# Kernel optimization log

Measured on AMD Instinct MI355X. Metric: run time of the kernel, lower is better.

Reference implementation:

```python
import jax, jax.numpy as jnp
import numpy as np

B, QDIM, KDIM, EMBED, HEADS = 8, 256, 256, 512, 8
HIMG, WIMG = 32, 32
HEAD_DIM = EMBED // HEADS


def setup_inputs() -> dict:
    key = jax.random.key(0)
    ks = jax.random.split(key, 8)
    scale_q = 1.0 / np.sqrt(QDIM)
    scale_k = 1.0 / np.sqrt(KDIM)
    return {
        "query": jax.random.normal(ks[0], (B, QDIM, HIMG, WIMG), jnp.float32),
        "key": jax.random.normal(ks[1], (B, KDIM, HIMG, WIMG), jnp.float32),
        "Wq": jax.random.uniform(ks[2], (EMBED, QDIM), jnp.float32, -scale_q, scale_q),
        "bq": jax.random.uniform(ks[3], (EMBED,), jnp.float32, -scale_q, scale_q),
        "Wk": jax.random.uniform(ks[4], (EMBED, KDIM), jnp.float32, -scale_k, scale_k),
        "bk": jax.random.uniform(ks[5], (EMBED,), jnp.float32, -scale_k, scale_k),
        "Wv": jax.random.uniform(ks[6], (EMBED, KDIM), jnp.float32, -scale_k, scale_k),
        "bv": jax.random.uniform(ks[7], (EMBED,), jnp.float32, -scale_k, scale_k),
    }


def reference(query, key, Wq, bq, Wk, bk, Wv, bv):
    b, _, h, w = query.shape
    s = h * w
    # (B, C, H, W) -> (B, S, C)
    q = query.transpose(0, 2, 3, 1).reshape(b, s, QDIM)
    kv = key.transpose(0, 2, 3, 1).reshape(b, s, KDIM)
    q = q @ Wq.T + bq            # (B, S, E)
    k = kv @ Wk.T + bk
    v = kv @ Wv.T + bv
    # split heads: (B, S, H, D) -> (B, H, S, D)
    q = q.reshape(b, s, HEADS, HEAD_DIM).transpose(0, 2, 1, 3)
    k = k.reshape(b, s, HEADS, HEAD_DIM).transpose(0, 2, 1, 3)
    v = v.reshape(b, s, HEADS, HEAD_DIM).transpose(0, 2, 1, 3)
    scores = jnp.einsum("bhqd,bhkd->bhqk", q, k) / np.sqrt(HEAD_DIM)
    # causal additive mask: -inf above the diagonal
    causal = jnp.tril(jnp.ones((s, s), dtype=bool))
    scores = jnp.where(causal, scores, -jnp.inf)
    attn = jax.nn.softmax(scores, axis=-1)
    x = jnp.einsum("bhqk,bhkd->bhqd", attn, v)   # (B, H, S, D)
    # (B, H, S, D) -> (B, H, D, S) -> (B, E, H_img, W_img)
    out = x.transpose(0, 1, 3, 2).reshape(b, EMBED, h, w)
    return out
```

## Files before the change

kernel.cpp:

```cpp
#include <hip/hip_runtime.h>
#include <hip/hip_bf16.h>

#define BATCH 8
#define CDIM 256
#define SEQ 1024
#define EMB 512
#define NHEAD 8
#define HDIM 64

typedef __bf16 bf16x8 __attribute__((ext_vector_type(8)));
typedef float f32x4 __attribute__((ext_vector_type(4)));
typedef float f32x16 __attribute__((ext_vector_type(16)));

static __device__ __forceinline__ unsigned short f2b(float f) {
    __hip_bfloat16 h = __float2bfloat16(f);
    return __builtin_bit_cast(unsigned short, h);
}

static __device__ __forceinline__ f32x4 mfma16(bf16x8 a, bf16x8 b, f32x4 c) {
    return __builtin_amdgcn_mfma_f32_16x16x32_bf16(a, b, c, 0, 0, 0);
}
static __device__ __forceinline__ f32x16 mfma32(bf16x8 a, bf16x8 b, f32x16 c) {
    return __builtin_amdgcn_mfma_f32_32x32x16_bf16(a, b, c, 0, 0, 0);
}

__global__ __launch_bounds__(256) void prep_w(
    const float* __restrict__ Wq, const float* __restrict__ Wk,
    const float* __restrict__ Wv, unsigned short* __restrict__ Wc)
{
    int pz = blockIdx.z;
    const float* W = (pz == 0) ? Wq : (pz == 1 ? Wk : Wv);
    int idx = (blockIdx.x * 256 + threadIdx.x) * 8;
    float4 v0 = *(const float4*)&W[idx];
    float4 v1 = *(const float4*)&W[idx + 4];
    int4 pk;
    pk.x = (int)((unsigned)f2b(v0.x) | ((unsigned)f2b(v0.y) << 16));
    pk.y = (int)((unsigned)f2b(v0.z) | ((unsigned)f2b(v0.w) << 16));
    pk.z = (int)((unsigned)f2b(v1.x) | ((unsigned)f2b(v1.y) << 16));
    pk.w = (int)((unsigned)f2b(v1.z) | ((unsigned)f2b(v1.w) << 16));
    *(int4*)&Wc[(size_t)pz * (EMB * CDIM) + idx] = pk;
}

__global__ __launch_bounds__(256) void transpose_cvt(
    const float* __restrict__ query, const float* __restrict__ key_,
    unsigned short* __restrict__ Xq, unsigned short* __restrict__ Xk)
{
    __shared__ alignas(16) unsigned short sT[64 * 66];
    int tid = threadIdx.x;
    int s0 = blockIdx.x * 64, c0 = blockIdx.y * 64;
    int z = blockIdx.z;
    int which = z >> 3, b = z & 7;
    const float* src = which ? key_ : query;
    unsigned short* dst = which ? Xk : Xq;

#pragma unroll
    for (int p = 0; p < 4; ++p) {
        int c = (tid >> 4) + p * 16;
        int sch = tid & 15;
        float4 v = *(const float4*)&src[((size_t)b * CDIM + c0 + c) * SEQ + s0 + sch * 4];
        sT[c * 66 + sch * 4 + 0] = f2b(v.x);
        sT[c * 66 + sch * 4 + 1] = f2b(v.y);
        sT[c * 66 + sch * 4 + 2] = f2b(v.z);
        sT[c * 66 + sch * 4 + 3] = f2b(v.w);
    }
    __syncthreads();
#pragma unroll
    for (int p = 0; p < 4; ++p) {
        int s = (tid >> 4) + p * 16;
        int cch = tid & 15;
        unsigned short e0 = sT[(cch * 4 + 0) * 66 + s];
        unsigned short e1 = sT[(cch * 4 + 1) * 66 + s];
        unsigned short e2 = sT[(cch * 4 + 2) * 66 + s];
        unsigned short e3 = sT[(cch * 4 + 3) * 66 + s];
        uint2 pk;
        pk.x = (unsigned)e0 | ((unsigned)e1 << 16);
        pk.y = (unsigned)e2 | ((unsigned)e3 << 16);
        *(uint2*)&dst[((size_t)b * SEQ + s0 + s) * CDIM + c0 + cch * 4] = pk;
    }
}

__global__ __launch_bounds__(256) void proj_kernel(
    const unsigned short* __restrict__ Xq, const unsigned short* __restrict__ Xk,
    const unsigned short* __restrict__ Wc,
    const float* __restrict__ bq, const float* __restrict__ bk,
    const float* __restrict__ bv,
    unsigned short* __restrict__ Qb, unsigned short* __restrict__ Kb,
    unsigned short* __restrict__ Vt)
{
    __shared__ alignas(16) unsigned short sA[128 * 72];
    __shared__ alignas(16) unsigned short sB[128 * 72];
    int tid = threadIdx.x;
    int n0 = blockIdx.x * 128;
    int m0 = blockIdx.y * 128;
    int proj = n0 >> 9;
    const unsigned short* X = (proj == 0) ? Xq : Xk;
    const float* bias = (proj == 0) ? bq : (proj == 1 ? bk : bv);

    int lane = tid & 63, w = tid >> 6;
    int l16 = lane & 15, lhi = lane >> 4;
    int wr = w >> 1, wc = w & 1;

    f32x4 zero = {0.f, 0.f, 0.f, 0.f};
    f32x4 acc[4][4];
#pragma unroll
    for (int i = 0; i < 4; ++i)
#pragma unroll
        for (int j = 0; j < 4; ++j) acc[i][j] = zero;

    for (int kt = 0; kt < 4; ++kt) {
        int c0 = kt * 64;
        if (kt) __syncthreads();
#pragma unroll
        for (int p = 0; p < 4; ++p) {
            int row = (tid >> 3) + p * 32, ch = tid & 7;
            *(int4*)&sA[row * 72 + ch * 8] =
                *(const int4*)&X[(size_t)(m0 + row) * CDIM + c0 + ch * 8];
            *(int4*)&sB[row * 72 + ch * 8] =
                *(const int4*)&Wc[(size_t)(n0 + row) * CDIM + c0 + ch * 8];
        }
        __syncthreads();
        const unsigned short* tA = (proj == 2) ? &sB[0] : &sA[0];
        const unsigned short* tB = (proj == 2) ? &sA[0] : &sB[0];
#pragma unroll
        for (int kk = 0; kk < 2; ++kk) {
            bf16x8 af[4], bfr[4];
#pragma unroll
            for (int i = 0; i < 4; ++i)
                af[i] = *(const bf16x8*)&tA[(wr * 64 + i * 16 + l16) * 72 + kk * 32 + lhi * 8];
#pragma unroll
            for (int j = 0; j < 4; ++j)
                bfr[j] = *(const bf16x8*)&tB[(wc * 64 + j * 16 + l16) * 72 + kk * 32 + lhi * 8];
#pragma unroll
            for (int i = 0; i < 4; ++i)
#pragma unroll
                for (int j = 0; j < 4; ++j)
                    acc[i][j] = mfma16(af[i], bfr[j], acc[i][j]);
        }
    }

    if (proj != 2) {
        unsigned short* dst = proj ? Kb : Qb;
        float scale = proj ? 1.0f : (0.125f * 1.44269504f);
#pragma unroll
        for (int i = 0; i < 4; ++i) {
#pragma unroll
            for (int j = 0; j < 4; ++j) {
                int e = (n0 & 511) + wc * 64 + j * 16 + l16;
                float bval = bias[e];
                int hh = e >> 6, dd = e & 63;
#pragma unroll
                for (int r = 0; r < 4; ++r) {
                    int mg = m0 + wr * 64 + i * 16 + lhi * 4 + r;
                    int bb = mg >> 10, s = mg & 1023;
                    dst[(((size_t)bb * NHEAD + hh) * SEQ + s) * HDIM + dd] =
                        f2b((acc[i][j][r] + bval) * scale);
                }
            }
        }
    } else {
#pragma unroll
        for (int i = 0; i < 4; ++i) {
#pragma unroll
            for (int r = 0; r < 4; ++r) {
                int e = (n0 & 511) + wr * 64 + i * 16 + lhi * 4 + r;
                float bval = bias[e];
                int hh = e >> 6, dd = e & 63;
#pragma unroll
                for (int j = 0; j < 4; ++j) {
                    int mg = m0 + wc * 64 + j * 16 + l16;
                    int bb = mg >> 10, s = mg & 1023;
                    Vt[(((size_t)bb * NHEAD + hh) * HDIM + dd) * SEQ + s] =
                        f2b(acc[i][j][r] + bval);
                }
            }
        }
    }
}

__global__ __launch_bounds__(64, 3) void attn_kernel(
    const unsigned short* __restrict__ Qb, const unsigned short* __restrict__ Kb,
    const unsigned short* __restrict__ Vt, float* __restrict__ out)
{
    int lane = threadIdx.x;
    int l32 = lane & 31, hi = lane >> 5;
    int bh = blockIdx.x;
    int qt = (int)(gridDim.y - 1 - blockIdx.y);
    int b = bh >> 3, h = bh & 7;
    int q0 = qt * 32;

    const unsigned short* Qhead = Qb + (size_t)bh * SEQ * HDIM;
    const unsigned short* Khead = Kb + (size_t)bh * SEQ * HDIM;
    const unsigned short* Vhead = Vt + (size_t)bh * HDIM * SEQ;

    bf16x8 qf[4];
#pragma unroll
    for (int dblk = 0; dblk < 4; ++dblk)
        qf[dblk] = *(const bf16x8*)&Qhead[(size_t)(q0 + l32) * HDIM + dblk * 16 + hi * 8];

    f32x16 o0, o1;
#pragma unroll
    for (int r = 0; r < 16; ++r) { o0[r] = 0.f; o1[r] = 0.f; }
    float m = -1e30f, l = 0.f;

    int nt = qt + 1;
    for (int kt = 0; kt < nt; ++kt) {
        int k0 = kt * 32;
        bf16x8 ka[4];
#pragma unroll
        for (int dblk = 0; dblk < 4; ++dblk)
            ka[dblk] = *(const bf16x8*)&Khead[(size_t)(k0 + l32) * HDIM + dblk * 16 + hi * 8];
        f32x16 st;
#pragma unroll
        for (int r = 0; r < 16; ++r) st[r] = 0.f;
#pragma unroll
        for (int dblk = 0; dblk < 4; ++dblk)
            st = mfma32(ka[dblk], qf[dblk], st);

        bf16x8 va[2][2];
#pragma unroll
        for (int t = 0; t < 2; ++t)
#pragma unroll
            for (int ks = 0; ks < 2; ++ks)
                va[t][ks] = *(const bf16x8*)
                    &Vhead[(size_t)(t * 32 + l32) * SEQ + k0 + ks * 16 + hi * 8];

        if (kt == qt) {
#pragma unroll
            for (int r = 0; r < 16; ++r) {
                int kk = (r & 3) + 8 * (r >> 2) + 4 * hi;
                if (kk > l32) st[r] = -1e38f;
            }
        }

        float tmax = st[0];
#pragma unroll
        for (int r = 1; r < 16; ++r) tmax = fmaxf(tmax, st[r]);
        tmax = fmaxf(tmax, __shfl_xor(tmax, 32));
        if (!__all(tmax <= m + 8.0f)) {
            float mnew = fmaxf(m, tmax);
            float corr = __builtin_amdgcn_exp2f(m - mnew);
#pragma unroll
            for (int r = 0; r < 16; ++r) { o0[r] *= corr; o1[r] *= corr; }
            l *= corr;
            m = mnew;
        }
        float p[16];
        float ts = 0.f;
#pragma unroll
        for (int r = 0; r < 16; ++r) {
            p[r] = __builtin_amdgcn_exp2f(st[r] - m);
            ts += p[r];
        }
        ts += __shfl_xor(ts, 32);
        l += ts;

        unsigned u[8];
#pragma unroll
        for (int i = 0; i < 8; ++i) {
            unsigned r_;
            asm("v_cvt_pk_bf16_f32 %0, %1, %2" : "=v"(r_) : "v"(p[2 * i]), "v"(p[2 * i + 1]));
            u[i] = r_;
        }
        asm("v_permlane32_swap_b32 %0, %1" : "+v"(u[0]), "+v"(u[2]));
        asm("v_permlane32_swap_b32 %0, %1" : "+v"(u[1]), "+v"(u[3]));
        asm("v_permlane32_swap_b32 %0, %1" : "+v"(u[4]), "+v"(u[6]));
        asm("v_permlane32_swap_b32 %0, %1" : "+v"(u[5]), "+v"(u[7]));
        uint4 pw0 = {u[0], u[1], u[2], u[3]};
        uint4 pw1 = {u[4], u[5], u[6], u[7]};
        bf16x8 pb0 = __builtin_bit_cast(bf16x8, pw0);
        bf16x8 pb1 = __builtin_bit_cast(bf16x8, pw1);

        o0 = mfma32(va[0][0], pb0, o0);
        o1 = mfma32(va[1][0], pb0, o1);
        o0 = mfma32(va[0][1], pb1, o0);
        o1 = mfma32(va[1][1], pb1, o1);
    }

    float inv = 1.0f / l;
    size_t base = ((size_t)b * EMB + h * HDIM) * SEQ + q0 + l32;
#pragma unroll
    for (int r = 0; r < 16; ++r) {
        int d0 = (r & 3) + 8 * (r >> 2) + 4 * hi;
        out[base + (size_t)d0 * SEQ] = o0[r] * inv;
        out[base + (size_t)(d0 + 32) * SEQ] = o1[r] * inv;
    }
}

extern "C" void kernel_launch(void* const* d_in, const int* in_sizes, int n_in,
                              void* d_out, int out_size, void* d_ws, size_t ws_size,
                              hipStream_t stream) {
    const float* query = (const float*)d_in[0];
    const float* key_  = (const float*)d_in[1];
    const float* Wq    = (const float*)d_in[2];
    const float* bq    = (const float*)d_in[3];
    const float* Wk    = (const float*)d_in[4];
    const float* bk    = (const float*)d_in[5];
    const float* Wv    = (const float*)d_in[6];
    const float* bv    = (const float*)d_in[7];
    float* out = (float*)d_out;

    char* ws = (char*)d_ws;
    unsigned short* Qb = (unsigned short*)(ws);
    unsigned short* Kb = (unsigned short*)(ws + 8388608);
    unsigned short* Vt = (unsigned short*)(ws + 16777216);
    unsigned short* Xq = (unsigned short*)(ws + 25165824);
    unsigned short* Xk = (unsigned short*)(ws + 29360128);
    unsigned short* Wc = (unsigned short*)((char*)d_out + 16777216 - 1048576);

    prep_w<<<dim3(64, 1, 3), 256, 0, stream>>>(Wq, Wk, Wv, Wc);
    transpose_cvt<<<dim3(SEQ / 64, CDIM / 64, 2 * BATCH), 256, 0, stream>>>(query, key_, Xq, Xk);
    proj_kernel<<<dim3(12, 64), 256, 0, stream>>>(Xq, Xk, Wc, bq, bk, bv, Qb, Kb, Vt);
    attn_kernel<<<dim3(BATCH * NHEAD, SEQ / 32), 64, 0, stream>>>(Qb, Kb, Vt, out);
}
```

Before: 139.9 us.

## Prefetch K/V tiles in registers and vectorize projection output stores

The attention loop now double-buffers the K and V fragments in registers. It loads tile kt+1 while computing tile kt, so global-load latency overlaps with MFMA and softmax work. The row max and row sum become tree reductions to shorten dependency chains. Launch bounds drop from 3 to 2 waves per SIMD so the extra live registers fit, which risks lower occupancy. In the projection kernel the MFMA operand roles are swapped so each lane holds 4 consecutive output elements, allowing packed 8-byte stores and a float4 bias load instead of scattered 2-byte stores.

```diff
diff --git a/kernel.cpp b/kernel.cpp
--- a/kernel.cpp
+++ b/kernel.cpp
@@ -87,8 +87,8 @@
     unsigned short* __restrict__ Qb, unsigned short* __restrict__ Kb,
     unsigned short* __restrict__ Vt)
 {
-    __shared__ alignas(16) unsigned short sA[128 * 72];
-    __shared__ alignas(16) unsigned short sB[128 * 72];
+    __shared__ alignas(16) unsigned short sX[128 * 72];
+    __shared__ alignas(16) unsigned short sW[128 * 72];
     int tid = threadIdx.x;
     int n0 = blockIdx.x * 128;
     int m0 = blockIdx.y * 128;
@@ -113,14 +113,14 @@
 #pragma unroll
         for (int p = 0; p < 4; ++p) {
             int row = (tid >> 3) + p * 32, ch = tid & 7;
-            *(int4*)&sA[row * 72 + ch * 8] =
+            *(int4*)&sX[row * 72 + ch * 8] =
                 *(const int4*)&X[(size_t)(m0 + row) * CDIM + c0 + ch * 8];
-            *(int4*)&sB[row * 72 + ch * 8] =
+            *(int4*)&sW[row * 72 + ch * 8] =
                 *(const int4*)&Wc[(size_t)(n0 + row) * CDIM + c0 + ch * 8];
         }
         __syncthreads();
-        const unsigned short* tA = (proj == 2) ? &sB[0] : &sA[0];
-        const unsigned short* tB = (proj == 2) ? &sA[0] : &sB[0];
+        const unsigned short* tA = (proj == 2) ? &sX[0] : &sW[0];
+        const unsigned short* tB = (proj == 2) ? &sW[0] : &sX[0];
 #pragma unroll
         for (int kk = 0; kk < 2; ++kk) {
             bf16x8 af[4], bfr[4];
@@ -143,41 +143,43 @@
         float scale = proj ? 1.0f : (0.125f * 1.44269504f);
 #pragma unroll
         for (int i = 0; i < 4; ++i) {
+            int e0 = (n0 & 511) + wr * 64 + i * 16 + lhi * 4;
+            float4 bv4 = *(const float4*)&bias[e0];
+            int hh = e0 >> 6, dd = e0 & 63;
 #pragma unroll
             for (int j = 0; j < 4; ++j) {
-                int e = (n0 & 511) + wc * 64 + j * 16 + l16;
-                float bval = bias[e];
-                int hh = e >> 6, dd = e & 63;
-#pragma unroll
-                for (int r = 0; r < 4; ++r) {
-                    int mg = m0 + wr * 64 + i * 16 + lhi * 4 + r;
-                    int bb = mg >> 10, s = mg & 1023;
-                    dst[(((size_t)bb * NHEAD + hh) * SEQ + s) * HDIM + dd] =
-                        f2b((acc[i][j][r] + bval) * scale);
-                }
+                int mg = m0 + wc * 64 + j * 16 + l16;
+                int bb = mg >> 10, s = mg & 1023;
+                uint2 pk;
+                pk.x = (unsigned)f2b((acc[i][j][0] + bv4.x) * scale) |
+                       ((unsigned)f2b((acc[i][j][1] + bv4.y) * scale) << 16);
+                pk.y = (unsigned)f2b((acc[i][j][2] + bv4.z) * scale) |
+                       ((unsigned)f2b((acc[i][j][3] + bv4.w) * scale) << 16);
+                *(uint2*)&dst[(((size_t)bb * NHEAD + hh) * SEQ + s) * HDIM + dd] = pk;
             }
         }
     } else {
 #pragma unroll
-        for (int i = 0; i < 4; ++i) {
-#pragma unroll
-            for (int r = 0; r < 4; ++r) {
-                int e = (n0 & 511) + wr * 64 + i * 16 + lhi * 4 + r;
-                float bval = bias[e];
-                int hh = e >> 6, dd = e & 63;
-#pragma unroll
-                for (int j = 0; j < 4; ++j) {
-                    int mg = m0 + wc * 64 + j * 16 + l16;
-                    int bb = mg >> 10, s = mg & 1023;
-                    Vt[(((size_t)bb * NHEAD + hh) * HDIM + dd) * SEQ + s] =
-                        f2b(acc[i][j][r] + bval);
-                }
+        for (int j = 0; j < 4; ++j) {
+            int e = (n0 & 511) + wc * 64 + j * 16 + l16;
+            float bval = bias[e];
+            int hh = e >> 6, dd = e & 63;
+#pragma unroll
+            for (int i = 0; i < 4; ++i) {
+                int mg = m0 + wr * 64 + i * 16 + lhi * 4;
+                int bb = mg >> 10, s = mg & 1023;
+                uint2 pk;
+                pk.x = (unsigned)f2b(acc[i][j][0] + bval) |
+                       ((unsigned)f2b(acc[i][j][1] + bval) << 16);
+                pk.y = (unsigned)f2b(acc[i][j][2] + bval) |
+                       ((unsigned)f2b(acc[i][j][3] + bval) << 16);
+                *(uint2*)&Vt[(((size_t)bb * NHEAD + hh) * HDIM + dd) * SEQ + s] = pk;
             }
         }
     }
 }
 
-__global__ __launch_bounds__(64, 3) void attn_kernel(
+__global__ __launch_bounds__(64, 2) void attn_kernel(
     const unsigned short* __restrict__ Qb, const unsigned short* __restrict__ Kb,
     const unsigned short* __restrict__ Vt, float* __restrict__ out)
 {
@@ -202,27 +204,26 @@
     for (int r = 0; r < 16; ++r) { o0[r] = 0.f; o1[r] = 0.f; }
     float m = -1e30f, l = 0.f;
 
-    int nt = qt + 1;
-    for (int kt = 0; kt < nt; ++kt) {
+    auto loadKV = [&](int kt, bf16x8 (&ka)[4], bf16x8 (&va)[2][2]) {
         int k0 = kt * 32;
-        bf16x8 ka[4];
 #pragma unroll
         for (int dblk = 0; dblk < 4; ++dblk)
             ka[dblk] = *(const bf16x8*)&Khead[(size_t)(k0 + l32) * HDIM + dblk * 16 + hi * 8];
-        f32x16 st;
-#pragma unroll
-        for (int r = 0; r < 16; ++r) st[r] = 0.f;
-#pragma unroll
-        for (int dblk = 0; dblk < 4; ++dblk)
-            st = mfma32(ka[dblk], qf[dblk], st);
-
-        bf16x8 va[2][2];
 #pragma unroll
         for (int t = 0; t < 2; ++t)
 #pragma unroll
             for (int ks = 0; ks < 2; ++ks)
                 va[t][ks] = *(const bf16x8*)
                     &Vhead[(size_t)(t * 32 + l32) * SEQ + k0 + ks * 16 + hi * 8];
+    };
+
+    auto compute = [&](int kt, const bf16x8 (&ka)[4], const bf16x8 (&va)[2][2]) {
+        f32x16 st;
+#pragma unroll
+        for (int r = 0; r < 16; ++r) st[r] = 0.f;
+#pragma unroll
+        for (int dblk = 0; dblk < 4; ++dblk)
+            st = mfma32(ka[dblk], qf[dblk], st);
 
         if (kt == qt) {
 #pragma unroll
@@ -232,9 +233,14 @@
             }
         }
 
-        float tmax = st[0];
-#pragma unroll
-        for (int r = 1; r < 16; ++r) tmax = fmaxf(tmax, st[r]);
+        float t8[8];
+#pragma unroll
+        for (int r = 0; r < 8; ++r) t8[r] = fmaxf(st[r], st[r + 8]);
+        float t4[4];
+#pragma unroll
+        for (int r = 0; r < 4; ++r) t4[r] = fmaxf(t8[r], t8[r + 4]);
+        float t2a = fmaxf(t4[0], t4[2]), t2b = fmaxf(t4[1], t4[3]);
+        float tmax = fmaxf(t2a, t2b);
         tmax = fmaxf(tmax, __shfl_xor(tmax, 32));
         if (!__all(tmax <= m + 8.0f)) {
             float mnew = fmaxf(m, tmax);
@@ -245,12 +251,15 @@
             m = mnew;
         }
         float p[16];
-        float ts = 0.f;
-#pragma unroll
-        for (int r = 0; r < 16; ++r) {
-            p[r] = __builtin_amdgcn_exp2f(st[r] - m);
-            ts += p[r];
-        }
+#pragma unroll
+        for (int r = 0; r < 16; ++r) p[r] = __builtin_amdgcn_exp2f(st[r] - m);
+        float s8[8];
+#pragma unroll
+        for (int r = 0; r < 8; ++r) s8[r] = p[r] + p[r + 8];
+        float s4[4];
+#pragma unroll
+        for (int r = 0; r < 4; ++r) s4[r] = s8[r] + s8[r + 4];
+        float ts = (s4[0] + s4[2]) + (s4[1] + s4[3]);
         ts += __shfl_xor(ts, 32);
         l += ts;
 
@@ -274,6 +283,19 @@
         o1 = mfma32(va[1][0], pb0, o1);
         o0 = mfma32(va[0][1], pb1, o0);
         o1 = mfma32(va[1][1], pb1, o1);
+    };
+
+    int nt = qt + 1;
+    bf16x8 kaA[4], vaA[2][2], kaB[4], vaB[2][2];
+    loadKV(0, kaA, vaA);
+    int kt = 0;
+    while (true) {
+        if (kt + 1 < nt) loadKV(kt + 1, kaB, vaB);
+        compute(kt, kaA, vaA);
+        if (++kt >= nt) break;
+        if (kt + 1 < nt) loadKV(kt + 1, kaA, vaA);
+        compute(kt, kaB, vaB);
+        if (++kt >= nt) break;
     }
 
     float inv = 1.0f / l;
```

New measurement: 140.9 us. About the same (+0.7%).
